# Performance work log

Hardware: AMD Instinct MI355X
Metric: run time of the kernel (lower is better)

## Reference

```python
import jax, jax.numpy as jnp
import numpy as np
import math

H = 128      # hidden_size
B = 4        # bsz
N = 32       # bsz * num_doc_per_q
L = 128      # doc_len


def setup_inputs() -> dict:
    key = jax.random.key(0)
    ks = jax.random.split(key, 7)
    word_ent_info = jax.random.normal(ks[0], (N, L, H), dtype=jnp.float32)
    word_ent_info_mask = jax.random.randint(ks[1], (N, L), 0, 2, dtype=jnp.int32)
    doc = jax.random.normal(ks[2], (N, L, H), dtype=jnp.float32)
    doc_mask = jax.random.randint(ks[3], (N, L), 0, 2, dtype=jnp.int32)
    q_for_text = jax.random.normal(ks[4], (B, H), dtype=jnp.float32)
    # nn.Linear(3H, H): weight [H, 3H], bias [H]
    W1 = jax.random.normal(ks[5], (H, 3 * H), dtype=jnp.float32) / math.sqrt(3 * H)
    b1 = jnp.zeros((H,), dtype=jnp.float32)
    # nn.Linear(H, 1): weight [1, H], bias [1]
    w2 = jax.random.normal(ks[6], (1, H), dtype=jnp.float32) / math.sqrt(H)
    b2 = jnp.zeros((1,), dtype=jnp.float32)
    return {"word_ent_info": word_ent_info, "word_ent_info_mask": word_ent_info_mask,
            "doc": doc, "doc_mask": doc_mask, "q_for_text": q_for_text,
            "W1": W1, "b1": b1, "w2": w2, "b2": b2}


def reference(word_ent_info, word_ent_info_mask, doc, doc_mask, q_for_text, W1, b1, w2, b2):
    n, l, h = doc.shape
    bsz = q_for_text.shape[0]
    dt = doc.dtype

    # word_ent_infoagg = mask^T @ word_ent_info -> [N, H]
    m = word_ent_info_mask.astype(dt)
    ent_agg = jnp.einsum('nl,nlh->nh', m, word_ent_info)

    # q expanded to one row per document: [N, H]
    q_exp = jnp.repeat(q_for_text, n // bsz, axis=0)

    # Split W1 over the concat([doc_self, ent_agg, q_agg]) feature axis.
    # score_pre[n,j,k,:] = W1a @ (doc_j*doc_k) + W1b @ (doc_j*ent_agg) + W1c @ (doc_k*q)
    W1a, W1b, W1c = jnp.split(W1, 3, axis=1)        # each [H, H]
    A = jnp.einsum('nje,nke,ge->njkg', doc, doc, W1a)          # [N,L,L,H]
    Bt = jnp.einsum('nje,ge->njg', doc * ent_agg[:, None, :], W1b)  # [N,L,H]
    Ct = jnp.einsum('nke,ge->nkg', doc * q_exp[:, None, :], W1c)    # [N,L,H]
    hid = jnp.tanh(A + Bt[:, :, None, :] + Ct[:, None, :, :] + b1)  # [N,L,L,H]

    score = (jnp.einsum('njkg,g->njk', hid, w2[0]) + b2[0]) / math.sqrt(h)

    dm = doc_mask.astype(dt)
    score_mask = dm[:, :, None] * dm[:, None, :]     # [N,L,L]
    score = jnp.where(score_mask == 0.0, jnp.asarray(-1e9, dt), score)
    w = jax.nn.softmax(score, axis=-1) * score_mask
    doc_ent_enc = jnp.einsum('njk,nkh->njh', w, doc)  # [N,L,H]
    return doc_ent_enc
```

## Files before the change

### kernel.cpp

```cpp
#include <hip/hip_runtime.h>
#include <hip/hip_bf16.h>
#include <math.h>

#define Hh 128
#define Nn 32
#define Ll 128
#define W1S 384
#define PAD 136

typedef __attribute__((ext_vector_type(8))) short short8;
typedef __attribute__((ext_vector_type(4))) float floatx4;

__device__ __forceinline__ unsigned short f2bf(float x) {
  __hip_bfloat16 h = __float2bfloat16(x);
  return __builtin_bit_cast(unsigned short, h);
}
__device__ __forceinline__ float bf2f(short s) {
  unsigned int u = ((unsigned int)(unsigned short)s) << 16;
  return __builtin_bit_cast(float, u);
}
__device__ __forceinline__ short8 pack8(float4 a, float4 b) {
  short8 r;
  r[0] = (short)f2bf(a.x); r[1] = (short)f2bf(a.y);
  r[2] = (short)f2bf(a.z); r[3] = (short)f2bf(a.w);
  r[4] = (short)f2bf(b.x); r[5] = (short)f2bf(b.y);
  r[6] = (short)f2bf(b.z); r[7] = (short)f2bf(b.w);
  return r;
}

__launch_bounds__(256, 2)
__global__ void k_prep(const float* __restrict__ wei, const int* __restrict__ wmask,
                       const float* __restrict__ doc, const float* __restrict__ q,
                       const float* __restrict__ W1, const float* __restrict__ b1,
                       float* __restrict__ Bt, float* __restrict__ Ct) {
  __shared__ __align__(16) short Wsb[Hh * PAD];
  __shared__ __align__(16) short docb[64 * PAD];
  __shared__ __align__(16) float red[2][Hh];
  __shared__ __align__(16) float scale[Hh];

  int b = blockIdx.x;
  int n = b >> 2, which = (b >> 1) & 1, mh = b & 1;
  int tid = threadIdx.x;
  const float* docn = doc + (size_t)n * Ll * Hh;
  int e8 = (tid & 15) * 8;

  float4 dreg[4][2];
#pragma unroll
  for (int p = 0; p < 4; ++p) {
    int row = mh * 64 + p * 16 + (tid >> 4);
    const float4* dp = (const float4*)(docn + (size_t)row * Hh + e8);
    dreg[p][0] = dp[0]; dreg[p][1] = dp[1];
  }
#pragma unroll
  for (int p = 0; p < 8; ++p) {
    int row = p * 16 + (tid >> 4);
    const float4* wp = (const float4*)(W1 + (size_t)row * W1S + (which + 1) * Hh + e8);
    *(short8*)(Wsb + row * PAD + e8) = pack8(wp[0], wp[1]);
  }
  if (which == 1) {
    if (tid < Hh) scale[tid] = q[(n >> 3) * Hh + tid];
  } else {
    int e = tid & 127, halfl = tid >> 7;
    const float* wp = wei + (size_t)n * Ll * Hh + (size_t)halfl * 64 * Hh + e;
    const int* mp = wmask + n * Ll + halfl * 64;
    float a = 0.f;
#pragma unroll 16
    for (int l = 0; l < 64; ++l) a = fmaf((float)mp[l], wp[(size_t)l * Hh], a);
    red[halfl][e] = a;
  }
  __syncthreads();
  if (which == 0 && tid < Hh) scale[tid] = red[0][tid] + red[1][tid];
  __syncthreads();
  {
    float s[8];
#pragma unroll
    for (int i = 0; i < 8; ++i) s[i] = scale[e8 + i];
#pragma unroll
    for (int p = 0; p < 4; ++p) {
      int r = p * 16 + (tid >> 4);
      float4 a = dreg[p][0], bq = dreg[p][1];
      a.x *= s[0]; a.y *= s[1]; a.z *= s[2]; a.w *= s[3];
      bq.x *= s[4]; bq.y *= s[5]; bq.z *= s[6]; bq.w *= s[7];
      *(short8*)(docb + r * PAD + e8) = pack8(a, bq);
    }
  }
  __syncthreads();

  int lane = tid & 63, w = tid >> 6;
  int l15 = lane & 15, quad = lane >> 4;
  floatx4 acc[8];
#pragma unroll
  for (int nt = 0; nt < 8; ++nt) acc[nt] = (floatx4){0.f, 0.f, 0.f, 0.f};
#pragma unroll
  for (int c = 0; c < 4; ++c) {
    int eo = c * 32 + quad * 8;
    short8 af = *(const short8*)(docb + (w * 16 + l15) * PAD + eo);
    short8 bfr[8];
#pragma unroll
    for (int nt = 0; nt < 8; ++nt)
      bfr[nt] = *(const short8*)(Wsb + (nt * 16 + l15) * PAD + eo);
#pragma unroll
    for (int nt = 0; nt < 8; ++nt)
      acc[nt] = __builtin_amdgcn_mfma_f32_16x16x32_bf16(af, bfr[nt], acc[nt], 0, 0, 0);
  }

  float* outp = (which ? Ct : Bt) + (size_t)n * Ll * Hh;
#pragma unroll
  for (int nt = 0; nt < 8; ++nt) {
    int g = nt * 16 + l15;
    float badd = which ? 0.f : b1[g];
#pragma unroll
    for (int r = 0; r < 4; ++r) {
      int k = mh * 64 + w * 16 + quad * 4 + r;
      outp[(size_t)k * Hh + g] = acc[nt][r] + badd;
    }
  }
}

__launch_bounds__(512, 4)
__global__ void k_main(const float* __restrict__ doc, const int* __restrict__ dmask,
                       const float* __restrict__ W1,
                       const float* __restrict__ w2, const float* __restrict__ b2,
                       const float* __restrict__ Bt, const float* __restrict__ Ct,
                       float* __restrict__ out) {
  __shared__ __align__(16) short As[Hh * PAD];
  __shared__ __align__(16) short docb[Hh * PAD];
  __shared__ __align__(16) float sc[4][Ll];
  __shared__ __align__(16) float scw[4][Ll];
  __shared__ int jl[Ll], ml[Ll], cnts[4];

  int bid = blockIdx.x;
  int n = bid & 31, t = bid >> 5;
  int tid = threadIdx.x;
  int lane = tid & 63, wv = tid >> 6;
  const float* docn = doc + (size_t)n * Ll * Hh;
  const int* dmn = dmask + n * Ll;

  int jme = -1, mflag = 0, pre = 0;
  if (wv < 2) {
    jme = (wv << 6) + lane;
    mflag = dmn[jme] != 0;
    unsigned long long bal = __ballot(mflag);
    pre = __popcll(bal & ((1ull << lane) - 1ull));
    if (lane == 0) { int tot = __popcll(bal); cnts[wv] = tot; cnts[2 + wv] = 64 - tot; }
  }
  __syncthreads();
  int cnt = cnts[0] + cnts[1];
  if (wv == 0) { if (mflag) jl[pre] = jme; else ml[lane - pre] = jme; }
  else if (wv == 1) { if (mflag) jl[cnts[0] + pre] = jme; else ml[cnts[2] + (lane - pre)] = jme; }
  __syncthreads();

  {
    int rr = tid >> 7, h = tid & 127;
    int mi = 4 * t + rr;
    if (mi < Ll - cnt) out[((size_t)n * Ll + ml[mi]) * Hh + h] = 0.f;
  }
  if (4 * t >= cnt) return;

  int e8 = (tid & 15) * 8;
#pragma unroll
  for (int p = 0; p < 4; ++p) {
    int row = p * 32 + (tid >> 4);
    const float4* wp = (const float4*)(W1 + (size_t)row * W1S + e8);
    *(short8*)(As + row * PAD + e8) = pack8(wp[0], wp[1]);
    const float4* dp = (const float4*)(docn + (size_t)row * Hh + e8);
    *(short8*)(docb + row * PAD + e8) = pack8(dp[0], dp[1]);
  }
  __syncthreads();

  int l15 = lane & 15, quad = lane >> 4;

  short8 draw[4];
#pragma unroll
  for (int c = 0; c < 4; ++c)
    draw[c] = *(const short8*)(docb + (wv * 16 + l15) * PAD + c * 32 + quad * 8);

  float w2r[8];
#pragma unroll
  for (int nt = 0; nt < 8; ++nt) w2r[nt] = w2[nt * 16 + l15];

  const float c2 = 2.885390081777927f;
  const float* ctn = Ct + (size_t)n * Ll * Hh;

  for (int jj = 0; jj < 4; ++jj) {
    int idx = 4 * t + jj;
    if (idx >= cnt) break;
    int j = jl[idx];
    const float* jrow = docn + (size_t)j * Hh;

    floatx4 acc[8];
#pragma unroll
    for (int nt = 0; nt < 8; ++nt) acc[nt] = (floatx4){0.f, 0.f, 0.f, 0.f};
#pragma unroll
    for (int c = 0; c < 4; ++c) {
      int eo = c * 32 + quad * 8;
      const float4* jp = (const float4*)(jrow + eo);
      float4 j0 = jp[0], j1 = jp[1];
      float4 ta, tb;
      ta.x = bf2f(draw[c][0]) * j0.x; ta.y = bf2f(draw[c][1]) * j0.y;
      ta.z = bf2f(draw[c][2]) * j0.z; ta.w = bf2f(draw[c][3]) * j0.w;
      tb.x = bf2f(draw[c][4]) * j1.x; tb.y = bf2f(draw[c][5]) * j1.y;
      tb.z = bf2f(draw[c][6]) * j1.z; tb.w = bf2f(draw[c][7]) * j1.w;
      short8 af = pack8(ta, tb);
#pragma unroll
      for (int nt = 0; nt < 8; ++nt) {
        short8 bfr = *(const short8*)(As + (nt * 16 + l15) * PAD + eo);
        acc[nt] = __builtin_amdgcn_mfma_f32_16x16x32_bf16(af, bfr, acc[nt], 0, 0, 0);
      }
    }

    float bbc[8];
    const float* btrow = Bt + ((size_t)n * Ll + j) * Hh;
#pragma unroll
    for (int nt = 0; nt < 8; ++nt) bbc[nt] = btrow[nt * 16 + l15] * c2;
#pragma unroll
    for (int r = 0; r < 4; ++r) {
      int k = wv * 16 + quad * 4 + r;
      const float* ctp = ctn + (size_t)k * Hh + l15;
      float p = 0.f;
#pragma unroll
      for (int nt = 0; nt < 8; ++nt) {
        float s = acc[nt][r] + ctp[nt * 16];
        float a2 = fmaf(s, c2, bbc[nt]);
        float e = exp2f(a2);
        float th = fmaf(-2.f, __builtin_amdgcn_rcpf(e + 1.f), 1.f);
        p = fmaf(th, w2r[nt], p);
      }
      p += __shfl_xor(p, 1);
      p += __shfl_xor(p, 2);
      p += __shfl_xor(p, 4);
      p += __shfl_xor(p, 8);
      if (l15 == 0) sc[jj][k] = p;
    }
  }
  __syncthreads();

  if (wv < 4) {
    int idx = 4 * t + wv;
    if (idx < cnt) {
      float b2v = b2[0];
      const float inv = 0.088388347648318447f;
      int m0 = dmn[lane], m1 = dmn[lane + 64];
      float s0 = (sc[wv][lane] + b2v) * inv;
      float s1 = (sc[wv][lane + 64] + b2v) * inv;
      s0 = m0 ? s0 : -1e9f;
      s1 = m1 ? s1 : -1e9f;
      float mx = fmaxf(s0, s1);
#pragma unroll
      for (int off = 32; off; off >>= 1) mx = fmaxf(mx, __shfl_xor(mx, off));
      float ex0 = __expf(s0 - mx), ex1 = __expf(s1 - mx);
      float sm = ex0 + ex1;
#pragma unroll
      for (int off = 32; off; off >>= 1) sm += __shfl_xor(sm, off);
      float rden = 1.f / sm;
      scw[wv][lane] = m0 ? ex0 * rden : 0.f;
      scw[wv][lane + 64] = m1 ? ex1 * rden : 0.f;
    } else {
      scw[wv][lane] = 0.f;
      scw[wv][lane + 64] = 0.f;
    }
  }
  __syncthreads();

  float* ored = (float*)As;
  {
    int halfk = tid >> 7, h = tid & 127;
    const float* dbase = docn + (size_t)halfk * 32 * Hh + h;
    float o0 = 0.f, o1 = 0.f, o2 = 0.f, o3 = 0.f;
#pragma unroll
    for (int k4 = 0; k4 < 8; ++k4) {
      float4 s0 = *(const float4*)&scw[0][halfk * 32 + k4 * 4];
      float4 s1 = *(const float4*)&scw[1][halfk * 32 + k4 * 4];
      float4 s2 = *(const float4*)&scw[2][halfk * 32 + k4 * 4];
      float4 s3 = *(const float4*)&scw[3][halfk * 32 + k4 * 4];
      float d0 = dbase[(size_t)(k4 * 4 + 0) * Hh];
      float d1 = dbase[(size_t)(k4 * 4 + 1) * Hh];
      float d2 = dbase[(size_t)(k4 * 4 + 2) * Hh];
      float d3 = dbase[(size_t)(k4 * 4 + 3) * Hh];
      o0 = fmaf(s0.x, d0, o0); o0 = fmaf(s0.y, d1, o0); o0 = fmaf(s0.z, d2, o0); o0 = fmaf(s0.w, d3, o0);
      o1 = fmaf(s1.x, d0, o1); o1 = fmaf(s1.y, d1, o1); o1 = fmaf(s1.z, d2, o1); o1 = fmaf(s1.w, d3, o1);
      o2 = fmaf(s2.x, d0, o2); o2 = fmaf(s2.y, d1, o2); o2 = fmaf(s2.z, d2, o2); o2 = fmaf(s2.w, d3, o2);
      o3 = fmaf(s3.x, d0, o3); o3 = fmaf(s3.y, d1, o3); o3 = fmaf(s3.z, d2, o3); o3 = fmaf(s3.w, d3, o3);
    }
    ored[(halfk * 4 + 0) * Hh + h] = o0;
    ored[(halfk * 4 + 1) * Hh + h] = o1;
    ored[(halfk * 4 + 2) * Hh + h] = o2;
    ored[(halfk * 4 + 3) * Hh + h] = o3;
  }
  __syncthreads();
  {
    int jj2 = tid >> 7, h = tid & 127;
    int idx = 4 * t + jj2;
    if (idx < cnt) {
      float v = ored[(0 * 4 + jj2) * Hh + h] + ored[(1 * 4 + jj2) * Hh + h] +
                ored[(2 * 4 + jj2) * Hh + h] + ored[(3 * 4 + jj2) * Hh + h];
      out[((size_t)n * Ll + jl[idx]) * Hh + h] = v;
    }
  }
}

extern "C" void kernel_launch(void* const* d_in, const int* in_sizes, int n_in,
                              void* d_out, int out_size, void* d_ws, size_t ws_size,
                              hipStream_t stream) {
  const float* wei   = (const float*)d_in[0];
  const int*   wmask = (const int*)d_in[1];
  const float* doc   = (const float*)d_in[2];
  const int*   dmask = (const int*)d_in[3];
  const float* q     = (const float*)d_in[4];
  const float* W1    = (const float*)d_in[5];
  const float* b1    = (const float*)d_in[6];
  const float* w2    = (const float*)d_in[7];
  const float* b2    = (const float*)d_in[8];
  float* out = (float*)d_out;

  float* ws = (float*)d_ws;
  float* Bt = ws;
  float* Ct = Bt + (size_t)Nn * Ll * Hh;

  k_prep<<<Nn * 4, 256, 0, stream>>>(wei, wmask, doc, q, W1, b1, Bt, Ct);
  k_main<<<Nn * 32, 512, 0, stream>>>(doc, dmask, W1, w2, b2, Bt, Ct, out);
}
```

Measured before the change: 130.5 us.

## Process eight query rows per block and keep Ct slice in registers

Each block of k_main now handles eight valid rows j instead of four, and the grid is halved to 16 blocks per document. The per-block setup (bf16 conversion of W1a and the doc tile into shared memory) is amortised over twice as many rows. The Ct values for each thread's k rows are loaded once into registers instead of being re-read for every j. The masked-row zeroing loop, the softmax stage and the final weighted-sum stage are widened to match. The cost is more registers per thread (32 extra floats for Ct plus eight accumulators), which may lower occupancy, and fewer blocks for parallelism.

```diff
diff --git a/kernel.cpp b/kernel.cpp
--- a/kernel.cpp
+++ b/kernel.cpp
@@ -125,8 +125,8 @@
                        float* __restrict__ out) {
   __shared__ __align__(16) short As[Hh * PAD];
   __shared__ __align__(16) short docb[Hh * PAD];
-  __shared__ __align__(16) float sc[4][Ll];
-  __shared__ __align__(16) float scw[4][Ll];
+  __shared__ __align__(16) float sc[8][Ll];
+  __shared__ __align__(16) float scw[8][Ll];
   __shared__ int jl[Ll], ml[Ll], cnts[4];
 
   int bid = blockIdx.x;
@@ -152,10 +152,11 @@
 
   {
     int rr = tid >> 7, h = tid & 127;
-    int mi = 4 * t + rr;
-    if (mi < Ll - cnt) out[((size_t)n * Ll + ml[mi]) * Hh + h] = 0.f;
-  }
-  if (4 * t >= cnt) return;
+    int mcnt = Ll - cnt;
+    for (int mi = 4 * t + rr; mi < mcnt; mi += 64)
+      out[((size_t)n * Ll + ml[mi]) * Hh + h] = 0.f;
+  }
+  if (8 * t >= cnt) return;
 
   int e8 = (tid & 15) * 8;
 #pragma unroll
@@ -179,11 +180,20 @@
 #pragma unroll
   for (int nt = 0; nt < 8; ++nt) w2r[nt] = w2[nt * 16 + l15];
 
+  const float* ctn = Ct + (size_t)n * Ll * Hh;
+  float ctv[4][8];
+#pragma unroll
+  for (int r = 0; r < 4; ++r) {
+    const float* ctp = ctn + (size_t)(wv * 16 + quad * 4 + r) * Hh + l15;
+#pragma unroll
+    for (int nt = 0; nt < 8; ++nt) ctv[r][nt] = ctp[nt * 16];
+  }
+
   const float c2 = 2.885390081777927f;
-  const float* ctn = Ct + (size_t)n * Ll * Hh;
-
-  for (int jj = 0; jj < 4; ++jj) {
-    int idx = 4 * t + jj;
+
+#pragma unroll 2
+  for (int jj = 0; jj < 8; ++jj) {
+    int idx = 8 * t + jj;
     if (idx >= cnt) break;
     int j = jl[idx];
     const float* jrow = docn + (size_t)j * Hh;
@@ -216,11 +226,10 @@
 #pragma unroll
     for (int r = 0; r < 4; ++r) {
       int k = wv * 16 + quad * 4 + r;
-      const float* ctp = ctn + (size_t)k * Hh + l15;
       float p = 0.f;
 #pragma unroll
       for (int nt = 0; nt < 8; ++nt) {
-        float s = acc[nt][r] + ctp[nt * 16];
+        float s = acc[nt][r] + ctv[r][nt];
         float a2 = fmaf(s, c2, bbc[nt]);
         float e = exp2f(a2);
         float th = fmaf(-2.f, __builtin_amdgcn_rcpf(e + 1.f), 1.f);
@@ -235,8 +244,8 @@
   }
   __syncthreads();
 
-  if (wv < 4) {
-    int idx = 4 * t + wv;
+  {
+    int idx = 8 * t + wv;
     if (idx < cnt) {
       float b2v = b2[0];
       const float inv = 0.088388347648318447f;
@@ -264,37 +273,41 @@
 
   float* ored = (float*)As;
   {
-    int halfk = tid >> 7, h = tid & 127;
-    const float* dbase = docn + (size_t)halfk * 32 * Hh + h;
-    float o0 = 0.f, o1 = 0.f, o2 = 0.f, o3 = 0.f;
+    int qk = tid >> 7, h = tid & 127;
+    const float* dbase = docn + (size_t)qk * 32 * Hh + h;
+    float o[8];
+#pragma unroll
+    for (int jj = 0; jj < 8; ++jj) o[jj] = 0.f;
 #pragma unroll
     for (int k4 = 0; k4 < 8; ++k4) {
-      float4 s0 = *(const float4*)&scw[0][halfk * 32 + k4 * 4];
-      float4 s1 = *(const float4*)&scw[1][halfk * 32 + k4 * 4];
-      float4 s2 = *(const float4*)&scw[2][halfk * 32 + k4 * 4];
-      float4 s3 = *(const float4*)&scw[3][halfk * 32 + k4 * 4];
       float d0 = dbase[(size_t)(k4 * 4 + 0) * Hh];
       float d1 = dbase[(size_t)(k4 * 4 + 1) * Hh];
       float d2 = dbase[(size_t)(k4 * 4 + 2) * Hh];
       float d3 = dbase[(size_t)(k4 * 4 + 3) * Hh];
-      o0 = fmaf(s0.x, d0, o0); o0 = fmaf(s0.y, d1, o0); o0 = fmaf(s0.z, d2, o0); o0 = fmaf(s0.w, d3, o0);
-      o1 = fmaf(s1.x, d0, o1); o1 = fmaf(s1.y, d1, o1); o1 = fmaf(s1.z, d2, o1); o1 = fmaf(s1.w, d3, o1);
-      o2 = fmaf(s2.x, d0, o2); o2 = fmaf(s2.y, d1, o2); o2 = fmaf(s2.z, d2, o2); o2 = fmaf(s2.w, d3, o2);
-      o3 = fmaf(s3.x, d0, o3); o3 = fmaf(s3.y, d1, o3); o3 = fmaf(s3.z, d2, o3); o3 = fmaf(s3.w, d3, o3);
-    }
-    ored[(halfk * 4 + 0) * Hh + h] = o0;
-    ored[(halfk * 4 + 1) * Hh + h] = o1;
-    ored[(halfk * 4 + 2) * Hh + h] = o2;
-    ored[(halfk * 4 + 3) * Hh + h] = o3;
-  }
-  __syncthreads();
-  {
-    int jj2 = tid >> 7, h = tid & 127;
-    int idx = 4 * t + jj2;
-    if (idx < cnt) {
-      float v = ored[(0 * 4 + jj2) * Hh + h] + ored[(1 * 4 + jj2) * Hh + h] +
-                ored[(2 * 4 + jj2) * Hh + h] + ored[(3 * 4 + jj2) * Hh + h];
-      out[((size_t)n * Ll + jl[idx]) * Hh + h] = v;
+#pragma unroll
+      for (int jj = 0; jj < 8; ++jj) {
+        float4 s = *(const float4*)&scw[jj][qk * 32 + k4 * 4];
+        o[jj] = fmaf(s.x, d0, o[jj]);
+        o[jj] = fmaf(s.y, d1, o[jj]);
+        o[jj] = fmaf(s.z, d2, o[jj]);
+        o[jj] = fmaf(s.w, d3, o[jj]);
+      }
+    }
+#pragma unroll
+    for (int jj = 0; jj < 8; ++jj) ored[(qk * 8 + jj) * Hh + h] = o[jj];
+  }
+  __syncthreads();
+  {
+    int h = tid & 127;
+#pragma unroll
+    for (int it = 0; it < 2; ++it) {
+      int jj2 = (tid >> 7) + it * 4;
+      int idx = 8 * t + jj2;
+      if (idx < cnt) {
+        float v = ored[(0 * 8 + jj2) * Hh + h] + ored[(1 * 8 + jj2) * Hh + h] +
+                  ored[(2 * 8 + jj2) * Hh + h] + ored[(3 * 8 + jj2) * Hh + h];
+        out[((size_t)n * Ll + jl[idx]) * Hh + h] = v;
+      }
     }
   }
 }
@@ -318,5 +331,5 @@
   float* Ct = Bt + (size_t)Nn * Ll * Hh;
 
   k_prep<<<Nn * 4, 256, 0, stream>>>(wei, wmask, doc, q, W1, b1, Bt, Ct);
-  k_main<<<Nn * 32, 512, 0, stream>>>(doc, dmask, W1, w2, b2, Bt, Ct, out);
-}
+  k_main<<<Nn * 16, 512, 0, stream>>>(doc, dmask, W1, w2, b2, Bt, Ct, out);
+}
```

Result: slower. 246.8 us (+89.2%).
